# Performance work log

Measured on AMD Instinct MI355X. Metric: run time of the kernel, lower is better.

The kernel has to match this reference:

```python
import jax, jax.numpy as jnp
import numpy as np

N_NODES = 50000
N_EDGES = 800000
D_IN, D_H, D_E = 512, 512, 256


def setup_inputs() -> dict:
    key = jax.random.key(0)
    ks = jax.random.split(key, 16)

    def lin(kw, kb, fan_in, fan_out):
        s = 1.0 / np.sqrt(fan_in)
        W = jax.random.uniform(kw, (fan_in, fan_out), dtype=jnp.float32, minval=-s, maxval=s)
        b = jax.random.uniform(kb, (fan_out,), dtype=jnp.float32, minval=-s, maxval=s)
        return W, b

    W1, b1 = lin(ks[2], ks[3], D_IN, D_H)
    W2, b2 = lin(ks[4], ks[5], D_H, D_H)
    W3, b3 = lin(ks[6], ks[7], D_H, D_E)
    We, be = lin(ks[8], ks[9], D_E, 7)
    Wh, bh = lin(ks[10], ks[11], D_E, 8)
    Wg, bg = lin(ks[12], ks[13], D_E, 57)

    return {
        "x": jax.random.normal(ks[0], (N_NODES, D_IN), dtype=jnp.float32),
        "edge_index": jax.random.randint(ks[1], (2, N_EDGES), 0, N_NODES, dtype=jnp.int32),
        "W1": W1, "b1": b1, "W2": W2, "b2": b2, "W3": W3, "b3": b3,
        "We": We, "be": be, "Wh": Wh, "bh": bh, "Wg": Wg, "bg": bg,
    }


def reference(x, edge_index, W1, b1, W2, b2, W3, b3, We, be, Wh, bh, Wg, bg):
    n = x.shape[0]
    # GCNConv: add self-loops, symmetric normalization D^{-1/2} A D^{-1/2}
    loops = jnp.arange(n, dtype=edge_index.dtype)
    src = jnp.concatenate([edge_index[0], loops])  # message sources
    dst = jnp.concatenate([edge_index[1], loops])  # aggregation targets
    deg = jax.ops.segment_sum(jnp.ones_like(src, dtype=x.dtype), dst, num_segments=n)
    dis = jnp.where(deg > 0, jax.lax.rsqrt(deg), 0.0)
    norm = (dis[src] * dis[dst])[:, None]  # [E+N, 1]

    def gcn_conv(h, W, b):
        h = h @ W                                   # [n, d_out]
        msg = h[src] * norm                         # gather + scale
        return jax.ops.segment_sum(msg, dst, num_segments=n) + b

    h = jax.nn.relu(gcn_conv(x, W1, b1))
    h = jax.nn.relu(gcn_conv(h, W2, b2))
    emb = gcn_conv(h, W3, b3)
    employment = emb @ We + be
    healthcare = emb @ Wh + bh
    grocery = emb @ Wg + bg
    return emb, employment, healthcare, grocery
```

## Files before the change

### kernel.cpp

```cpp
#include <hip/hip_runtime.h>

#define NN   50000
#define NNP  50048
#define NE   800000
#define DIN  512
#define DH   512
#define DE   256

#define CSR_CAP 1150016

typedef __bf16 bf16_t;
typedef __bf16 bf16x4 __attribute__((ext_vector_type(4)));
typedef __bf16 bf16x8 __attribute__((ext_vector_type(8)));
typedef float  f32x4  __attribute__((ext_vector_type(4)));
typedef _Float16 half_t;
typedef _Float16 half8 __attribute__((ext_vector_type(8)));

#define PB_SPLIT 25024
#define PB_IDEG  3125
#define PB_CSR   1124
#define PB_W1    1024
#define PB_W2    1024
#define PB_W3    512
#define PB_HEADW 80
#define PB_TOTAL (PB_SPLIT + PB_IDEG + PB_CSR + PB_W1 + PB_W2 + PB_W3 + PB_HEADW)

__global__ void k_prep(const float* __restrict__ X, bf16_t* __restrict__ Xh,
                       bf16_t* __restrict__ Xl, const int* __restrict__ dst,
                       int* __restrict__ indeg, int* __restrict__ csr,
                       const float* __restrict__ W1, bf16_t* __restrict__ B1h, bf16_t* __restrict__ B1l,
                       const float* __restrict__ W2, half_t* __restrict__ B2h, half_t* __restrict__ B2l,
                       const float* __restrict__ W3, half_t* __restrict__ B3h, half_t* __restrict__ B3l,
                       const float* __restrict__ We, const float* __restrict__ be,
                       const float* __restrict__ Wh, const float* __restrict__ bh,
                       const float* __restrict__ Wg, const float* __restrict__ bg,
                       bf16_t* __restrict__ Wth, bf16_t* __restrict__ Wtl,
                       float* __restrict__ bc) {
    int b = blockIdx.x;
    if (b < PB_SPLIT) {
        long idx = (long)b * 256 + threadIdx.x;
        long base = idx * 4;
        int row = (int)(base >> 9);
        f32x4 v;
        if (row < NN) v = *(const f32x4*)(X + base);
        else { v[0] = 0.f; v[1] = 0.f; v[2] = 0.f; v[3] = 0.f; }
        bf16x4 h, l;
        #pragma unroll
        for (int c = 0; c < 4; ++c) {
            float f = v[c];
            bf16_t hh = (bf16_t)f;
            h[c] = hh;
            l[c] = (bf16_t)(f - (float)hh);
        }
        *(bf16x4*)(Xh + base) = h;
        *(bf16x4*)(Xl + base) = l;
        return;
    }
    b -= PB_SPLIT;
    if (b < PB_IDEG) {
        int i = b * 256 + threadIdx.x;
        atomicAdd(&indeg[dst[i]], 1);
        return;
    }
    b -= PB_IDEG;
    if (b < PB_CSR) {
        int i = b * 256 + threadIdx.x;
        if (i < CSR_CAP / 4) ((int4*)csr)[i] = make_int4(NN, NN, NN, NN);
        return;
    }
    b -= PB_CSR;
    if (b < PB_W1) {
        int idx = b * 256 + threadIdx.x;
        int k = idx >> 9, n = idx & 511;
        float f = W1[idx];
        bf16_t h = (bf16_t)f;
        B1h[(size_t)n * DIN + k] = h;
        B1l[(size_t)n * DIN + k] = (bf16_t)(f - (float)h);
        return;
    }
    b -= PB_W1;
    if (b < PB_W2) {
        int idx = b * 256 + threadIdx.x;
        int k = idx >> 9, n = idx & 511;
        float f = W2[idx];
        half_t h = (half_t)f;
        B2h[(size_t)n * DH + k] = h;
        B2l[(size_t)n * DH + k] = (half_t)((f - (float)h) * 4096.f);
        return;
    }
    b -= PB_W2;
    if (b < PB_W3) {
        int idx = b * 256 + threadIdx.x;
        int k = idx >> 8, n = idx & 255;
        float f = W3[idx];
        half_t h = (half_t)f;
        B3h[(size_t)n * DH + k] = h;
        B3l[(size_t)n * DH + k] = (half_t)((f - (float)h) * 4096.f);
        return;
    }
    b -= PB_W3;
    {
        int idx = b * 256 + threadIdx.x;
        int n = idx / 256, k = idx % 256;
        float f = 0.f;
        if (n < 7)       f = We[k * 7 + n];
        else if (n < 15) f = Wh[k * 8 + (n - 7)];
        else if (n < 72) f = Wg[k * 57 + (n - 15)];
        bf16_t h = (bf16_t)f;
        Wth[idx] = h;
        Wtl[idx] = (bf16_t)(f - (float)h);
        if (k == 0) {
            float bb = 0.f;
            if (n < 7)       bb = be[n];
            else if (n < 15) bb = bh[n - 7];
            else if (n < 72) bb = bg[n - 15];
            bc[n] = bb;
        }
    }
}

#define SCAN_BLOCKS 49

__global__ __launch_bounds__(1024) void k_scan_a(const int* __restrict__ indeg,
                                                 int* __restrict__ rowptr,
                                                 float* __restrict__ dis,
                                                 int* __restrict__ bsum) {
    __shared__ int wsum[16];
    const int tid = threadIdx.x, lane = tid & 63, wid = tid >> 6;
    const int i = blockIdx.x * 1024 + tid;
    int deg = (i < NN) ? indeg[i] : 0;
    int v = (deg + 7) & ~7;
    int x = v;
    #pragma unroll
    for (int d = 1; d < 64; d <<= 1) {
        int t = __shfl_up(x, d, 64);
        if (lane >= d) x += t;
    }
    if (lane == 63) wsum[wid] = x;
    __syncthreads();
    if (wid == 0) {
        int s = (lane < 16) ? wsum[lane] : 0;
        #pragma unroll
        for (int d = 1; d < 16; d <<= 1) {
            int t = __shfl_up(s, d, 64);
            if (lane >= d) s += t;
        }
        if (lane < 16) wsum[lane] = s;
    }
    __syncthreads();
    int woff = (wid > 0) ? wsum[wid - 1] : 0;
    if (i < NN) {
        rowptr[i] = x - v + woff;
        dis[i] = rsqrtf((float)(deg + 1));
    } else if (i < NNP) {
        dis[i] = 0.f;
    }
    if (tid == 0) bsum[blockIdx.x] = wsum[15];
}

__global__ __launch_bounds__(64) void k_scan_b(const int* __restrict__ bsum,
                                               int* __restrict__ boff,
                                               int* __restrict__ rowptr) {
    const int lane = threadIdx.x;
    int v = (lane < SCAN_BLOCKS) ? bsum[lane] : 0;
    int x = v;
    #pragma unroll
    for (int d = 1; d < 64; d <<= 1) {
        int t = __shfl_up(x, d, 64);
        if (lane >= d) x += t;
    }
    if (lane < SCAN_BLOCKS) boff[lane] = x - v;
    if (lane == SCAN_BLOCKS - 1) rowptr[NN] = x;
}

__global__ void k_scan_c(const int* __restrict__ boff, int* __restrict__ rowptr,
                         int* __restrict__ cursor) {
    int i = blockIdx.x * blockDim.x + threadIdx.x;
    if (i < NN) {
        int r = rowptr[i] + boff[i >> 10];
        rowptr[i] = r;
        cursor[i] = r;
    }
}

__global__ void k_fill(const int* __restrict__ src, const int* __restrict__ dst,
                       int* __restrict__ cursor, int* __restrict__ csr, int e) {
    int i = blockIdx.x * blockDim.x + threadIdx.x;
    if (i < e) {
        int d = dst[i];
        int p = atomicAdd(&cursor[d], 1);
        csr[p] = src[i];
    }
}


__device__ __forceinline__ void gld_lds16(const void* g, void* l) {
    __builtin_amdgcn_global_load_lds(
        (const __attribute__((address_space(1))) unsigned int*)g,
        (__attribute__((address_space(3))) unsigned int*)l, 16, 0, 0);
}



__global__ __launch_bounds__(256) void k_gemm_bf3(
    const bf16_t* __restrict__ Ah, const bf16_t* __restrict__ Al,
    const bf16_t* __restrict__ Bh, const bf16_t* __restrict__ Bl,
    const float* __restrict__ disv,
    half_t* __restrict__ C, int N, int K) {
    __shared__ alignas(16) bf16_t sAh[128 * 32];
    __shared__ alignas(16) bf16_t sAl[128 * 32];
    __shared__ alignas(16) bf16_t sBh[128 * 32];
    __shared__ alignas(16) bf16_t sBl[128 * 32];

    const int tid = threadIdx.x;
    const int wave = tid >> 6, lane = tid & 63;
    const int quad = lane >> 4, l16 = lane & 15;
    const int bm = blockIdx.y * 128, bn = blockIdx.x * 128;
    const int wm = (wave & 1) * 64, wn = (wave >> 1) * 64;

    f32x4 acc[4][4];
    #pragma unroll
    for (int i = 0; i < 4; ++i)
        #pragma unroll
        for (int j = 0; j < 4; ++j)
            #pragma unroll
            for (int r = 0; r < 4; ++r) acc[i][j][r] = 0.f;

    const int srow = wave * 32 + (lane >> 2);
    const int schk = (((lane & 3) ^ ((lane >> 3) & 3))) * 16;
    char* lds0A = (char*)sAh + wave * 32 * 64;
    char* lds0a = (char*)sAl + wave * 32 * 64;
    char* lds0B = (char*)sBh + wave * 32 * 64;
    char* lds0b = (char*)sBl + wave * 32 * 64;

    const char* gAh0 = (const char*)(Ah + (size_t)(bm + srow) * K) + schk;
    const char* gAl0 = (const char*)(Al + (size_t)(bm + srow) * K) + schk;
    const char* gBh0 = (const char*)(Bh + (size_t)(bn + srow) * K) + schk;
    const char* gBl0 = (const char*)(Bl + (size_t)(bn + srow) * K) + schk;
    const size_t rstep = (size_t)16 * K * 2;

    const int rsw = (l16 >> 1) & 3;

    for (int k0 = 0; k0 < K; k0 += 32) {
        const size_t kb = (size_t)k0 * 2;
        gld_lds16(gAh0 + kb,         lds0A);
        gld_lds16(gAh0 + kb + rstep, lds0A + 1024);
        gld_lds16(gAl0 + kb,         lds0a);
        gld_lds16(gAl0 + kb + rstep, lds0a + 1024);
        gld_lds16(gBh0 + kb,         lds0B);
        gld_lds16(gBh0 + kb + rstep, lds0B + 1024);
        gld_lds16(gBl0 + kb,         lds0b);
        gld_lds16(gBl0 + kb + rstep, lds0b + 1024);
        __syncthreads();

        bf16x8 fah[4], fal[4], fbh[4], fbl[4];
        #pragma unroll
        for (int i = 0; i < 4; ++i) {
            fah[i] = *(const bf16x8*)(sAh + (wm + 16 * i + l16) * 32 + (quad ^ rsw) * 8);
            fal[i] = *(const bf16x8*)(sAl + (wm + 16 * i + l16) * 32 + (quad ^ rsw) * 8);
            fbh[i] = *(const bf16x8*)(sBh + (wn + 16 * i + l16) * 32 + (quad ^ rsw) * 8);
            fbl[i] = *(const bf16x8*)(sBl + (wn + 16 * i + l16) * 32 + (quad ^ rsw) * 8);
        }
        #pragma unroll
        for (int i = 0; i < 4; ++i)
            #pragma unroll
            for (int j = 0; j < 4; ++j) {
                acc[i][j] = __builtin_amdgcn_mfma_f32_16x16x32_bf16(fah[i], fbh[j], acc[i][j], 0, 0, 0);
                acc[i][j] = __builtin_amdgcn_mfma_f32_16x16x32_bf16(fah[i], fbl[j], acc[i][j], 0, 0, 0);
                acc[i][j] = __builtin_amdgcn_mfma_f32_16x16x32_bf16(fal[i], fbh[j], acc[i][j], 0, 0, 0);
            }
        __syncthreads();
    }

    #pragma unroll
    for (int i = 0; i < 4; ++i) {
        const int rowb = bm + wm + 16 * i + quad * 4;
        float d0 = disv[rowb], d1 = disv[rowb + 1], d2 = disv[rowb + 2], d3 = disv[rowb + 3];
        #pragma unroll
        for (int j = 0; j < 4; ++j) {
            int col = bn + wn + 16 * j + l16;
            C[(size_t)(rowb + 0) * N + col] = (half_t)(acc[i][j][0] * d0);
            C[(size_t)(rowb + 1) * N + col] = (half_t)(acc[i][j][1] * d1);
            C[(size_t)(rowb + 2) * N + col] = (half_t)(acc[i][j][2] * d2);
            C[(size_t)(rowb + 3) * N + col] = (half_t)(acc[i][j][3] * d3);
        }
    }
}


__global__ __launch_bounds__(512) void k_gemm_f16(
    const half_t* __restrict__ A,
    const half_t* __restrict__ Bh, const half_t* __restrict__ Bl,
    const float* __restrict__ disv,
    half_t* __restrict__ C, int N, int K) {
    __shared__ alignas(16) half_t sA [128 * 32];
    __shared__ alignas(16) half_t sBh[128 * 32];
    __shared__ alignas(16) half_t sBl[128 * 32];

    const int tid = threadIdx.x;
    const int wave = tid >> 6, lane = tid & 63;
    const int quad = lane >> 4, l16 = lane & 15;
    const int bm = blockIdx.y * 128, bn = blockIdx.x * 128;
    const int wm = (wave >> 1) * 32, wn = (wave & 1) * 64;

    f32x4 aH[2][4], aM[2][4];
    #pragma unroll
    for (int i = 0; i < 2; ++i)
        #pragma unroll
        for (int j = 0; j < 4; ++j)
            #pragma unroll
            for (int r = 0; r < 4; ++r) { aH[i][j][r] = 0.f; aM[i][j][r] = 0.f; }

    const int srow = wave * 16 + (lane >> 2);
    const int schk = (((lane & 3) ^ ((lane >> 3) & 3))) * 16;
    char* ldsA = (char*)sA  + wave * 1024;
    char* ldsB = (char*)sBh + wave * 1024;
    char* ldsb = (char*)sBl + wave * 1024;

    const char* gA0  = (const char*)(A  + (size_t)(bm + srow) * K) + schk;
    const char* gBh0 = (const char*)(Bh + (size_t)(bn + srow) * K) + schk;
    const char* gBl0 = (const char*)(Bl + (size_t)(bn + srow) * K) + schk;

    const int rsw = (l16 >> 1) & 3;

    for (int k0 = 0; k0 < K; k0 += 32) {
        const size_t kb = (size_t)k0 * 2;
        gld_lds16(gA0  + kb, ldsA);
        gld_lds16(gBh0 + kb, ldsB);
        gld_lds16(gBl0 + kb, ldsb);
        __syncthreads();

        half8 fa[2], fbh[4], fbl[4];
        #pragma unroll
        for (int i = 0; i < 2; ++i)
            fa[i] = *(const half8*)(sA + (wm + 16 * i + l16) * 32 + (quad ^ rsw) * 8);
        #pragma unroll
        for (int j = 0; j < 4; ++j) {
            fbh[j] = *(const half8*)(sBh + (wn + 16 * j + l16) * 32 + (quad ^ rsw) * 8);
            fbl[j] = *(const half8*)(sBl + (wn + 16 * j + l16) * 32 + (quad ^ rsw) * 8);
        }
        #pragma unroll
        for (int i = 0; i < 2; ++i)
            #pragma unroll
            for (int j = 0; j < 4; ++j) {
                aH[i][j] = __builtin_amdgcn_mfma_f32_16x16x32_f16(fa[i], fbh[j], aH[i][j], 0, 0, 0);
                aM[i][j] = __builtin_amdgcn_mfma_f32_16x16x32_f16(fa[i], fbl[j], aM[i][j], 0, 0, 0);
            }
        __syncthreads();
    }

    const float s = 1.f / 4096.f;
    #pragma unroll
    for (int i = 0; i < 2; ++i) {
        const int rowb = bm + wm + 16 * i + quad * 4;
        float d0 = disv[rowb], d1 = disv[rowb + 1], d2 = disv[rowb + 2], d3 = disv[rowb + 3];
        #pragma unroll
        for (int j = 0; j < 4; ++j) {
            int col = bn + wn + 16 * j + l16;
            C[(size_t)(rowb + 0) * N + col] = (half_t)(fmaf(aM[i][j][0], s, aH[i][j][0]) * d0);
            C[(size_t)(rowb + 1) * N + col] = (half_t)(fmaf(aM[i][j][1], s, aH[i][j][1]) * d1);
            C[(size_t)(rowb + 2) * N + col] = (half_t)(fmaf(aM[i][j][2], s, aH[i][j][2]) * d2);
            C[(size_t)(rowb + 3) * N + col] = (half_t)(fmaf(aM[i][j][3], s, aH[i][j][3]) * d3);
        }
    }
}


__global__ __launch_bounds__(128) void k_agg16(
    const half_t* __restrict__ t, const int* __restrict__ rowptr,
    const int* __restrict__ csr, const float* __restrict__ dis,
    const float* __restrict__ bias, half_t* __restrict__ out) {
    const int node = blockIdx.x * 2 + (threadIdx.x >> 6);
    const int lane = threadIdx.x & 63;
    const int beg = rowptr[node], end = rowptr[node + 1];
    const float din = dis[node];
    const char* tc = (const char*)t;
    const unsigned lb = (unsigned)lane * 16u;

    float a0[8], a1[8], a2[8], a3[8];
    #pragma unroll
    for (int c = 0; c < 8; ++c) { a0[c] = 0.f; a1[c] = 0.f; a2[c] = 0.f; a3[c] = 0.f; }

    if (beg < end) {
        int4 sa = *(const int4*)(csr + beg);
        int4 sb = *(const int4*)(csr + beg + 4);
        half8 v0 = *(const half8*)(tc + (((unsigned)sa.x) << 10) + lb);
        half8 v1 = *(const half8*)(tc + (((unsigned)sa.y) << 10) + lb);
        half8 v2 = *(const half8*)(tc + (((unsigned)sa.z) << 10) + lb);
        half8 v3 = *(const half8*)(tc + (((unsigned)sa.w) << 10) + lb);
        half8 v4 = *(const half8*)(tc + (((unsigned)sb.x) << 10) + lb);
        half8 v5 = *(const half8*)(tc + (((unsigned)sb.y) << 10) + lb);
        half8 v6 = *(const half8*)(tc + (((unsigned)sb.z) << 10) + lb);
        half8 v7 = *(const half8*)(tc + (((unsigned)sb.w) << 10) + lb);
        int4 na = sa, nb = sb;
        if (beg + 8 < end) {
            na = *(const int4*)(csr + beg + 8);
            nb = *(const int4*)(csr + beg + 12);
        }
        for (int e = beg; e < end; ) {
            half8 u0 = v0, u1 = v1, u2 = v2, u3 = v3, u4 = v4, u5 = v5, u6 = v6, u7 = v7;
            e += 8;
            if (e < end) {
                v0 = *(const half8*)(tc + (((unsigned)na.x) << 10) + lb);
                v1 = *(const half8*)(tc + (((unsigned)na.y) << 10) + lb);
                v2 = *(const half8*)(tc + (((unsigned)na.z) << 10) + lb);
                v3 = *(const half8*)(tc + (((unsigned)na.w) << 10) + lb);
                v4 = *(const half8*)(tc + (((unsigned)nb.x) << 10) + lb);
                v5 = *(const half8*)(tc + (((unsigned)nb.y) << 10) + lb);
                v6 = *(const half8*)(tc + (((unsigned)nb.z) << 10) + lb);
                v7 = *(const half8*)(tc + (((unsigned)nb.w) << 10) + lb);
                if (e + 8 < end) {
                    na = *(const int4*)(csr + e + 8);
                    nb = *(const int4*)(csr + e + 12);
                }
            }
            #pragma unroll
            for (int c = 0; c < 8; ++c) {
                a0[c] = fmaf((float)u0[c], din, a0[c]);
                a1[c] = fmaf((float)u1[c], din, a1[c]);
                a2[c] = fmaf((float)u2[c], din, a2[c]);
                a3[c] = fmaf((float)u3[c], din, a3[c]);
                a0[c] = fmaf((float)u4[c], din, a0[c]);
                a1[c] = fmaf((float)u5[c], din, a1[c]);
                a2[c] = fmaf((float)u6[c], din, a2[c]);
                a3[c] = fmaf((float)u7[c], din, a3[c]);
            }
        }
    }

    half8 sv = ((const half8*)(t + (size_t)node * DH))[lane];
    f32x4 bv0 = ((const f32x4*)bias)[lane * 2];
    f32x4 bv1 = ((const f32x4*)bias)[lane * 2 + 1];
    half8 h;
    #pragma unroll
    for (int c = 0; c < 8; ++c) {
        float b = (c < 4) ? bv0[c] : bv1[c - 4];
        float acc = (a0[c] + a1[c]) + (a2[c] + a3[c]);
        float o = fmaf((float)sv[c], din, acc) + b;
        o = fmaxf(o, 0.f);
        h[c] = (half_t)o;
    }
    *(half8*)(out + (size_t)node * DH + lane * 8) = h;
}

__global__ __launch_bounds__(128) void k_agg_f32(
    const half_t* __restrict__ t, const int* __restrict__ rowptr,
    const int* __restrict__ csr, const float* __restrict__ dis,
    const float* __restrict__ bias, float* __restrict__ out,
    bf16_t* __restrict__ Eh, bf16_t* __restrict__ El) {
    const int node = blockIdx.x * 4 + (threadIdx.x >> 5);
    const int lane = threadIdx.x & 31;
    const int beg = rowptr[node], end = rowptr[node + 1];
    const float din = dis[node];
    const char* tc = (const char*)t;
    const unsigned lb = (unsigned)lane * 16u;

    float a0[8], a1[8], a2[8], a3[8];
    #pragma unroll
    for (int c = 0; c < 8; ++c) { a0[c] = 0.f; a1[c] = 0.f; a2[c] = 0.f; a3[c] = 0.f; }

    if (beg < end) {
        int4 sa = *(const int4*)(csr + beg);
        int4 sb = *(const int4*)(csr + beg + 4);
        half8 v0 = *(const half8*)(tc + (((unsigned)sa.x) << 9) + lb);
        half8 v1 = *(const half8*)(tc + (((unsigned)sa.y) << 9) + lb);
        half8 v2 = *(const half8*)(tc + (((unsigned)sa.z) << 9) + lb);
        half8 v3 = *(const half8*)(tc + (((unsigned)sa.w) << 9) + lb);
        half8 v4 = *(const half8*)(tc + (((unsigned)sb.x) << 9) + lb);
        half8 v5 = *(const half8*)(tc + (((unsigned)sb.y) << 9) + lb);
        half8 v6 = *(const half8*)(tc + (((unsigned)sb.z) << 9) + lb);
        half8 v7 = *(const half8*)(tc + (((unsigned)sb.w) << 9) + lb);
        int4 na = sa, nb = sb;
        if (beg + 8 < end) {
            na = *(const int4*)(csr + beg + 8);
            nb = *(const int4*)(csr + beg + 12);
        }
        for (int e = beg; e < end; ) {
            half8 u0 = v0, u1 = v1, u2 = v2, u3 = v3, u4 = v4, u5 = v5, u6 = v6, u7 = v7;
            e += 8;
            if (e < end) {
                v0 = *(const half8*)(tc + (((unsigned)na.x) << 9) + lb);
                v1 = *(const half8*)(tc + (((unsigned)na.y) << 9) + lb);
                v2 = *(const half8*)(tc + (((unsigned)na.z) << 9) + lb);
                v3 = *(const half8*)(tc + (((unsigned)na.w) << 9) + lb);
                v4 = *(const half8*)(tc + (((unsigned)nb.x) << 9) + lb);
                v5 = *(const half8*)(tc + (((unsigned)nb.y) << 9) + lb);
                v6 = *(const half8*)(tc + (((unsigned)nb.z) << 9) + lb);
                v7 = *(const half8*)(tc + (((unsigned)nb.w) << 9) + lb);
                if (e + 8 < end) {
                    na = *(const int4*)(csr + e + 8);
                    nb = *(const int4*)(csr + e + 12);
                }
            }
            #pragma unroll
            for (int c = 0; c < 8; ++c) {
                a0[c] = fmaf((float)u0[c], din, a0[c]);
                a1[c] = fmaf((float)u1[c], din, a1[c]);
                a2[c] = fmaf((float)u2[c], din, a2[c]);
                a3[c] = fmaf((float)u3[c], din, a3[c]);
                a0[c] = fmaf((float)u4[c], din, a0[c]);
                a1[c] = fmaf((float)u5[c], din, a1[c]);
                a2[c] = fmaf((float)u6[c], din, a2[c]);
                a3[c] = fmaf((float)u7[c], din, a3[c]);
            }
        }
    }

    half8 sv = ((const half8*)(t + (size_t)node * DE))[lane];
    f32x4 bv0 = ((const f32x4*)bias)[lane * 2];
    f32x4 bv1 = ((const f32x4*)bias)[lane * 2 + 1];
    f32x4 o0, o1;
    bf16x8 hh, ll;
    #pragma unroll
    for (int c = 0; c < 8; ++c) {
        float b = (c < 4) ? bv0[c] : bv1[c - 4];
        float acc = (a0[c] + a1[c]) + (a2[c] + a3[c]);
        float o = fmaf((float)sv[c], din, acc) + b;
        if (c < 4) o0[c] = o; else o1[c - 4] = o;
        bf16_t h = (bf16_t)o;
        hh[c] = h;
        ll[c] = (bf16_t)(o - (float)h);
    }
    ((f32x4*)(out + (size_t)node * DE))[lane * 2]     = o0;
    ((f32x4*)(out + (size_t)node * DE))[lane * 2 + 1] = o1;
    *(bf16x8*)(Eh + (size_t)node * DE + lane * 8) = hh;
    *(bf16x8*)(El + (size_t)node * DE + lane * 8) = ll;
}


__global__ __launch_bounds__(256) void k_heads_mfma(
    const bf16_t* __restrict__ Eh, const bf16_t* __restrict__ El,
    const bf16_t* __restrict__ Wth, const bf16_t* __restrict__ Wtl,
    const float* __restrict__ bc,
    float* __restrict__ oe, float* __restrict__ oh, float* __restrict__ og) {
    const int wave = threadIdx.x >> 6, lane = threadIdx.x & 63;
    const int quad = lane >> 4, l16 = lane & 15;
    const int row0 = blockIdx.x * 64 + wave * 16;

    f32x4 acc[5];
    #pragma unroll
    for (int j = 0; j < 5; ++j)
        #pragma unroll
        for (int r = 0; r < 4; ++r) acc[j][r] = 0.f;

    const size_t abase = (size_t)(row0 + l16) * 256 + quad * 8;
    #pragma unroll
    for (int ks = 0; ks < 256; ks += 32) {
        bf16x8 ah = *(const bf16x8*)(Eh + abase + ks);
        bf16x8 al = *(const bf16x8*)(El + abase + ks);
        #pragma unroll
        for (int j = 0; j < 5; ++j) {
            const size_t bbase = (size_t)(j * 16 + l16) * 256 + ks + quad * 8;
            bf16x8 bh = *(const bf16x8*)(Wth + bbase);
            bf16x8 bl = *(const bf16x8*)(Wtl + bbase);
            acc[j] = __builtin_amdgcn_mfma_f32_16x16x32_bf16(ah, bh, acc[j], 0, 0, 0);
            acc[j] = __builtin_amdgcn_mfma_f32_16x16x32_bf16(ah, bl, acc[j], 0, 0, 0);
            acc[j] = __builtin_amdgcn_mfma_f32_16x16x32_bf16(al, bh, acc[j], 0, 0, 0);
        }
    }

    #pragma unroll
    for (int j = 0; j < 5; ++j) {
        int col = j * 16 + l16;
        if (col < 72) {
            float b = bc[col];
            #pragma unroll
            for (int r = 0; r < 4; ++r) {
                int row = row0 + quad * 4 + r;
                if (row < NN) {
                    float v = acc[j][r] + b;
                    if (col < 7)       oe[(size_t)row * 7 + col] = v;
                    else if (col < 15) oh[(size_t)row * 8 + (col - 7)] = v;
                    else               og[(size_t)row * 57 + (col - 15)] = v;
                }
            }
        }
    }
}


extern "C" void kernel_launch(void* const* d_in, const int* in_sizes, int n_in,
                              void* d_out, int out_size, void* d_ws, size_t ws_size,
                              hipStream_t stream) {
    const float* x   = (const float*)d_in[0];
    const int*   ei  = (const int*)d_in[1];
    const float* W1  = (const float*)d_in[2];
    const float* b1  = (const float*)d_in[3];
    const float* W2  = (const float*)d_in[4];
    const float* b2  = (const float*)d_in[5];
    const float* W3  = (const float*)d_in[6];
    const float* b3  = (const float*)d_in[7];
    const float* We  = (const float*)d_in[8];
    const float* be  = (const float*)d_in[9];
    const float* Wh  = (const float*)d_in[10];
    const float* bh  = (const float*)d_in[11];
    const float* Wg  = (const float*)d_in[12];
    const float* bg  = (const float*)d_in[13];

    const int* e_src = ei;
    const int* e_dst = ei + NE;

    half_t* buf0 = (half_t*)d_ws;
    half_t* buf1 = buf0 + (size_t)NNP * DH;
    bf16_t* Xh   = (bf16_t*)buf1;
    bf16_t* Xl   = Xh + (size_t)NNP * DH;
    bf16_t* embh = Xl;
    bf16_t* embl = embh + (size_t)NNP * DE;
    bf16_t* B1h  = Xl + (size_t)NNP * DH;
    bf16_t* B1l  = B1h + (size_t)DIN * DH;
    half_t* B2h  = (half_t*)(B1l + (size_t)DIN * DH);
    half_t* B2l  = B2h + (size_t)DH * DH;
    half_t* B3h  = B2l + (size_t)DH * DH;
    half_t* B3l  = B3h + (size_t)DE * DH;
    bf16_t* Wth  = (bf16_t*)(B3l + (size_t)DE * DH);
    bf16_t* Wtl  = Wth + 80 * 256;
    float*  bc   = (float*)(Wtl + 80 * 256);
    int*   indeg  = (int*)(bc + 128);
    int*   rowptr = indeg + 50048;
    int*   cursor = rowptr + 50048;
    float* dis    = (float*)(cursor + 50048);
    int*   csr    = (int*)(dis + 50048);
    int*   bsum   = csr + CSR_CAP;
    int*   boff   = bsum + 64;

    float* emb   = (float*)d_out;
    float* out_e = emb + (size_t)NN * DE;
    float* out_h = out_e + (size_t)NN * 7;
    float* out_g = out_h + (size_t)NN * 8;

    hipMemsetAsync(indeg, 0, NN * sizeof(int), stream);
    k_prep<<<PB_TOTAL, 256, 0, stream>>>(x, Xh, Xl, e_dst, indeg, csr,
                                         W1, B1h, B1l, W2, B2h, B2l, W3, B3h, B3l,
                                         We, be, Wh, bh, Wg, bg, Wth, Wtl, bc);
    k_scan_a<<<SCAN_BLOCKS, 1024, 0, stream>>>(indeg, rowptr, dis, bsum);
    k_scan_b<<<1, 64, 0, stream>>>(bsum, boff, rowptr);
    k_scan_c<<<(NN + 255) / 256, 256, 0, stream>>>(boff, rowptr, cursor);
    k_fill<<<(NE + 255) / 256, 256, 0, stream>>>(e_src, e_dst, cursor, csr, NE);

    const int gy = NNP / 128;

    k_gemm_bf3<<<dim3(DH / 128, gy), 256, 0, stream>>>(Xh, Xl, B1h, B1l, dis, buf0, DH, DIN);
    k_agg16<<<NN / 2, 128, 0, stream>>>(buf0, rowptr, csr, dis, b1, buf1);

    k_gemm_f16<<<dim3(DH / 128, gy), 512, 0, stream>>>(buf1, B2h, B2l, dis, buf0, DH, DH);
    k_agg16<<<NN / 2, 128, 0, stream>>>(buf0, rowptr, csr, dis, b2, buf1);

    k_gemm_f16<<<dim3(DE / 128, gy), 512, 0, stream>>>(buf1, B3h, B3l, dis, buf0, DE, DH);
    k_agg_f32<<<NN / 4, 128, 0, stream>>>(buf0, rowptr, csr, dis, b3, emb, embh, embl);

    k_heads_mfma<<<NNP / 64, 256, 0, stream>>>(embh, embl, Wth, Wtl, bc, out_e, out_h, out_g);
}
```

Measured before the change: 835.2 us.

## Double-buffer LDS tiles in GEMMs and widen bf3 GEMM to 512 threads

Both GEMM kernels now keep two LDS buffers and issue the global-to-LDS loads for the next K-step before computing on the current one, so load latency overlaps with MFMA work. The bf16x3 GEMM goes from 256 to 512 threads, with each wave owning a 32x64 sub-tile, which cuts accumulator registers per thread. The aggregation kernels' output stores become nontemporal. Doubled LDS use may lower occupancy. There is also a possible hazard: the loop's trailing sync is not visible here, and if it was dropped, the buffer being overwritten could race with reads of it.

```diff
diff --git a/kernel.cpp b/kernel.cpp
--- a/kernel.cpp
+++ b/kernel.cpp
@@ -202,67 +202,71 @@
 
 
 
-__global__ __launch_bounds__(256) void k_gemm_bf3(
+__global__ __launch_bounds__(512) void k_gemm_bf3(
     const bf16_t* __restrict__ Ah, const bf16_t* __restrict__ Al,
     const bf16_t* __restrict__ Bh, const bf16_t* __restrict__ Bl,
     const float* __restrict__ disv,
     half_t* __restrict__ C, int N, int K) {
-    __shared__ alignas(16) bf16_t sAh[128 * 32];
-    __shared__ alignas(16) bf16_t sAl[128 * 32];
-    __shared__ alignas(16) bf16_t sBh[128 * 32];
-    __shared__ alignas(16) bf16_t sBl[128 * 32];
+    __shared__ alignas(16) bf16_t sAh[2][128 * 32];
+    __shared__ alignas(16) bf16_t sAl[2][128 * 32];
+    __shared__ alignas(16) bf16_t sBh[2][128 * 32];
+    __shared__ alignas(16) bf16_t sBl[2][128 * 32];
 
     const int tid = threadIdx.x;
     const int wave = tid >> 6, lane = tid & 63;
     const int quad = lane >> 4, l16 = lane & 15;
     const int bm = blockIdx.y * 128, bn = blockIdx.x * 128;
-    const int wm = (wave & 1) * 64, wn = (wave >> 1) * 64;
-
-    f32x4 acc[4][4];
-    #pragma unroll
-    for (int i = 0; i < 4; ++i)
+    const int wm = (wave >> 1) * 32, wn = (wave & 1) * 64;
+
+    f32x4 acc[2][4];
+    #pragma unroll
+    for (int i = 0; i < 2; ++i)
         #pragma unroll
         for (int j = 0; j < 4; ++j)
             #pragma unroll
             for (int r = 0; r < 4; ++r) acc[i][j][r] = 0.f;
 
-    const int srow = wave * 32 + (lane >> 2);
-    const int schk = (((lane & 3) ^ ((lane >> 3) & 3))) * 16;
-    char* lds0A = (char*)sAh + wave * 32 * 64;
-    char* lds0a = (char*)sAl + wave * 32 * 64;
-    char* lds0B = (char*)sBh + wave * 32 * 64;
-    char* lds0b = (char*)sBl + wave * 32 * 64;
+    const int srow = tid >> 2;
+    const int schk = ((tid & 3) ^ ((tid >> 3) & 3)) * 16;
+    const unsigned ldso = (unsigned)wave * 1024;
 
     const char* gAh0 = (const char*)(Ah + (size_t)(bm + srow) * K) + schk;
     const char* gAl0 = (const char*)(Al + (size_t)(bm + srow) * K) + schk;
     const char* gBh0 = (const char*)(Bh + (size_t)(bn + srow) * K) + schk;
     const char* gBl0 = (const char*)(Bl + (size_t)(bn + srow) * K) + schk;
-    const size_t rstep = (size_t)16 * K * 2;
 
     const int rsw = (l16 >> 1) & 3;
-
-    for (int k0 = 0; k0 < K; k0 += 32) {
-        const size_t kb = (size_t)k0 * 2;
-        gld_lds16(gAh0 + kb,         lds0A);
-        gld_lds16(gAh0 + kb + rstep, lds0A + 1024);
-        gld_lds16(gAl0 + kb,         lds0a);
-        gld_lds16(gAl0 + kb + rstep, lds0a + 1024);
-        gld_lds16(gBh0 + kb,         lds0B);
-        gld_lds16(gBh0 + kb + rstep, lds0B + 1024);
-        gld_lds16(gBl0 + kb,         lds0b);
-        gld_lds16(gBl0 + kb + rstep, lds0b + 1024);
-        __syncthreads();
-
-        bf16x8 fah[4], fal[4], fbh[4], fbl[4];
-        #pragma unroll
-        for (int i = 0; i < 4; ++i) {
-            fah[i] = *(const bf16x8*)(sAh + (wm + 16 * i + l16) * 32 + (quad ^ rsw) * 8);
-            fal[i] = *(const bf16x8*)(sAl + (wm + 16 * i + l16) * 32 + (quad ^ rsw) * 8);
-            fbh[i] = *(const bf16x8*)(sBh + (wn + 16 * i + l16) * 32 + (quad ^ rsw) * 8);
-            fbl[i] = *(const bf16x8*)(sBl + (wn + 16 * i + l16) * 32 + (quad ^ rsw) * 8);
-        }
-        #pragma unroll
-        for (int i = 0; i < 4; ++i)
+    const int nsteps = K >> 5;
+
+    gld_lds16(gAh0, (char*)sAh[0] + ldso);
+    gld_lds16(gAl0, (char*)sAl[0] + ldso);
+    gld_lds16(gBh0, (char*)sBh[0] + ldso);
+    gld_lds16(gBl0, (char*)sBl[0] + ldso);
+    __syncthreads();
+
+    for (int t = 0; t < nsteps; ++t) {
+        const int cur = t & 1;
+        if (t + 1 < nsteps) {
+            const size_t kb = (size_t)(t + 1) * 64;
+            const int nx = cur ^ 1;
+            gld_lds16(gAh0 + kb, (char*)sAh[nx] + ldso);
+            gld_lds16(gAl0 + kb, (char*)sAl[nx] + ldso);
+            gld_lds16(gBh0 + kb, (char*)sBh[nx] + ldso);
+            gld_lds16(gBl0 + kb, (char*)sBl[nx] + ldso);
+        }
+        bf16x8 fah[2], fal[2], fbh[4], fbl[4];
+        #pragma unroll
+        for (int i = 0; i < 2; ++i) {
+            fah[i] = *(const bf16x8*)(sAh[cur] + (wm + 16 * i + l16) * 32 + (quad ^ rsw) * 8);
+            fal[i] = *(const bf16x8*)(sAl[cur] + (wm + 16 * i + l16) * 32 + (quad ^ rsw) * 8);
+        }
+        #pragma unroll
+        for (int j = 0; j < 4; ++j) {
+            fbh[j] = *(const bf16x8*)(sBh[cur] + (wn + 16 * j + l16) * 32 + (quad ^ rsw) * 8);
+            fbl[j] = *(const bf16x8*)(sBl[cur] + (wn + 16 * j + l16) * 32 + (quad ^ rsw) * 8);
+        }
+        #pragma unroll
+        for (int i = 0; i < 2; ++i)
             #pragma unroll
             for (int j = 0; j < 4; ++j) {
                 acc[i][j] = __builtin_amdgcn_mfma_f32_16x16x32_bf16(fah[i], fbh[j], acc[i][j], 0, 0, 0);
@@ -273,7 +277,7 @@
     }
 
     #pragma unroll
-    for (int i = 0; i < 4; ++i) {
+    for (int i = 0; i < 2; ++i) {
         const int rowb = bm + wm + 16 * i + quad * 4;
         float d0 = disv[rowb], d1 = disv[rowb + 1], d2 = disv[rowb + 2], d3 = disv[rowb + 3];
         #pragma unroll
@@ -293,9 +297,9 @@
     const half_t* __restrict__ Bh, const half_t* __restrict__ Bl,
     const float* __restrict__ disv,
     half_t* __restrict__ C, int N, int K) {
-    __shared__ alignas(16) half_t sA [128 * 32];
-    __shared__ alignas(16) half_t sBh[128 * 32];
-    __shared__ alignas(16) half_t sBl[128 * 32];
+    __shared__ alignas(16) half_t sA [2][128 * 32];
+    __shared__ alignas(16) half_t sBh[2][128 * 32];
+    __shared__ alignas(16) half_t sBl[2][128 * 32];
 
     const int tid = threadIdx.x;
     const int wave = tid >> 6, lane = tid & 63;
@@ -311,33 +315,39 @@
             #pragma unroll
             for (int r = 0; r < 4; ++r) { aH[i][j][r] = 0.f; aM[i][j][r] = 0.f; }
 
-    const int srow = wave * 16 + (lane >> 2);
-    const int schk = (((lane & 3) ^ ((lane >> 3) & 3))) * 16;
-    char* ldsA = (char*)sA  + wave * 1024;
-    char* ldsB = (char*)sBh + wave * 1024;
-    char* ldsb = (char*)sBl + wave * 1024;
+    const int srow = tid >> 2;
+    const int schk = ((tid & 3) ^ ((tid >> 3) & 3)) * 16;
+    const unsigned ldso = (unsigned)wave * 1024;
 
     const char* gA0  = (const char*)(A  + (size_t)(bm + srow) * K) + schk;
     const char* gBh0 = (const char*)(Bh + (size_t)(bn + srow) * K) + schk;
     const char* gBl0 = (const char*)(Bl + (size_t)(bn + srow) * K) + schk;
 
     const int rsw = (l16 >> 1) & 3;
-
-    for (int k0 = 0; k0 < K; k0 += 32) {
-        const size_t kb = (size_t)k0 * 2;
-        gld_lds16(gA0  + kb, ldsA);
-        gld_lds16(gBh0 + kb, ldsB);
-        gld_lds16(gBl0 + kb, ldsb);
-        __syncthreads();
-
+    const int nsteps = K >> 5;
+
+    gld_lds16(gA0,  (char*)sA[0]  + ldso);
+    gld_lds16(gBh0, (char*)sBh[0] + ldso);
+    gld_lds16(gBl0, (char*)sBl[0] + ldso);
+    __syncthreads();
+
+    for (int t = 0; t < nsteps; ++t) {
+        const int cur = t & 1;
+        if (t + 1 < nsteps) {
+            const size_t kb = (size_t)(t + 1) * 64;
+            const int nx = cur ^ 1;
+            gld_lds16(gA0  + kb, (char*)sA[nx]  + ldso);
+            gld_lds16(gBh0 + kb, (char*)sBh[nx] + ldso);
+            gld_lds16(gBl0 + kb, (char*)sBl[nx] + ldso);
+        }
         half8 fa[2], fbh[4], fbl[4];
         #pragma unroll
         for (int i = 0; i < 2; ++i)
-            fa[i] = *(const half8*)(sA + (wm + 16 * i + l16) * 32 + (quad ^ rsw) * 8);
+            fa[i] = *(const half8*)(sA[cur] + (wm + 16 * i + l16) * 32 + (quad ^ rsw) * 8);
         #pragma unroll
         for (int j = 0; j < 4; ++j) {
-            fbh[j] = *(const half8*)(sBh + (wn + 16 * j + l16) * 32 + (quad ^ rsw) * 8);
-            fbl[j] = *(const half8*)(sBl + (wn + 16 * j + l16) * 32 + (quad ^ rsw) * 8);
+            fbh[j] = *(const half8*)(sBh[cur] + (wn + 16 * j + l16) * 32 + (quad ^ rsw) * 8);
+            fbl[j] = *(const half8*)(sBl[cur] + (wn + 16 * j + l16) * 32 + (quad ^ rsw) * 8);
         }
         #pragma unroll
         for (int i = 0; i < 2; ++i)
@@ -440,7 +450,7 @@
         o = fmaxf(o, 0.f);
         h[c] = (half_t)o;
     }
-    *(half8*)(out + (size_t)node * DH + lane * 8) = h;
+    __builtin_nontemporal_store(h, (half8*)(out + (size_t)node * DH + lane * 8));
 }
 
 __global__ __launch_bounds__(128) void k_agg_f32(
@@ -521,8 +531,8 @@
         hh[c] = h;
         ll[c] = (bf16_t)(o - (float)h);
     }
-    ((f32x4*)(out + (size_t)node * DE))[lane * 2]     = o0;
-    ((f32x4*)(out + (size_t)node * DE))[lane * 2 + 1] = o1;
+    __builtin_nontemporal_store(o0, &((f32x4*)(out + (size_t)node * DE))[lane * 2]);
+    __builtin_nontemporal_store(o1, &((f32x4*)(out + (size_t)node * DE))[lane * 2 + 1]);
     *(bf16x8*)(Eh + (size_t)node * DE + lane * 8) = hh;
     *(bf16x8*)(El + (size_t)node * DE + lane * 8) = ll;
 }
@@ -639,7 +649,7 @@
 
     const int gy = NNP / 128;
 
-    k_gemm_bf3<<<dim3(DH / 128, gy), 256, 0, stream>>>(Xh, Xl, B1h, B1l, dis, buf0, DH, DIN);
+    k_gemm_bf3<<<dim3(DH / 128, gy), 512, 0, stream>>>(Xh, Xl, B1h, B1l, dis, buf0, DH, DIN);
     k_agg16<<<NN / 2, 128, 0, stream>>>(buf0, rowptr, csr, dis, b1, buf1);
 
     k_gemm_f16<<<dim3(DH / 128, gy), 512, 0, stream>>>(buf1, B2h, B2l, dis, buf0, DH, DH);
```

Result: no change. 835.6 us (+0.0%).
